# Kernel optimization log

Hardware: AMD Instinct MI355X
Metric: run time of the kernel (lower is better)

## Reference

```python
import jax, jax.numpy as jnp
import numpy as np

B, S, H = 32, 2048, 1024


def setup_inputs() -> dict:
    key = jax.random.key(0)
    k1, k2, k3, k4, k5, k6 = jax.random.split(key, 6)
    scale = 1.0 / np.sqrt(H)
    return {
        "query": jax.random.normal(k1, (B, 1, H), dtype=jnp.float32),
        "encoder_outputs": jax.random.normal(k2, (B, S, H), dtype=jnp.float32),
        "src_lengths": jax.random.randint(k3, (B,), 0, S, dtype=jnp.int64),
        "W_h": jax.random.normal(k4, (H, H), dtype=jnp.float32) * scale,
        "W_s": jax.random.normal(k5, (H, H), dtype=jnp.float32) * scale,
        "v": jax.random.normal(k6, (H,), dtype=jnp.float32) * scale,
    }


def reference(query, encoder_outputs, src_lengths, W_h, W_s, v):
    # score(h_i, s) = v^T tanh(W_h h_i + W_s s)
    proj_h = jnp.einsum("bsh,hd->bsd", encoder_outputs, W_h)   # (B,S,H)
    proj_s = jnp.einsum("bqh,hd->bqd", query, W_s)             # (B,1,H)
    scores = jnp.einsum("bsd,d->bs", jnp.tanh(proj_h + proj_s), v)  # (B,S)
    # sequence mask: True for valid positions
    mask = jnp.arange(encoder_outputs.shape[1])[None, :] < src_lengths[:, None]
    scores = jnp.where(mask, scores, -1e9)
    attn_weights = jax.nn.softmax(scores, axis=1)              # (B,S)
    attn_out = jnp.einsum("bs,bsh->bh", attn_weights, encoder_outputs)
    return attn_out[:, None, :]  # (B,1,H)
```

## Files before the change

### kernel.cpp

```cpp
#include <hip/hip_runtime.h>
#include <hip/hip_bf16.h>
#include <stdint.h>

#define NB 32
#define NS 2048
#define NH 1024

typedef __attribute__((ext_vector_type(8))) unsigned short ushort8v;
typedef __attribute__((ext_vector_type(4))) unsigned short ushort4v;
typedef __attribute__((ext_vector_type(8))) __bf16 bf16x8;
typedef __attribute__((ext_vector_type(4))) float floatx4;

__device__ __forceinline__ unsigned short f2bf(float f) {
    union { float f; unsigned int u; } x; x.f = f;
    unsigned int r = x.u + 0x7fffu + ((x.u >> 16) & 1u);
    return (unsigned short)(r >> 16);
}
__device__ __forceinline__ float bf2f(unsigned short u) {
    union { unsigned int u; float f; } x; x.u = ((unsigned int)u) << 16;
    return x.f;
}
__device__ __forceinline__ float tanh_fast(float x) {
    float e2 = __expf(2.0f * x);
    return 1.0f - 2.0f * __builtin_amdgcn_rcpf(e2 + 1.0f);
}
__device__ __forceinline__ void gload_lds16(const void* g, void* l) {
    __builtin_amdgcn_global_load_lds(
        (const __attribute__((address_space(1))) unsigned int*)g,
        (__attribute__((address_space(3))) unsigned int*)l, 16, 0, 0);
}

__global__ void prep_kernel(const float* __restrict__ E,
                            const int* __restrict__ lens,
                            unsigned short* __restrict__ Ebf,
                            const float* __restrict__ Wh,
                            unsigned short* __restrict__ WhP,
                            const float* __restrict__ q,
                            const float* __restrict__ Ws,
                            float* __restrict__ projs)
{
    const int bid = blockIdx.x;
    const int t   = threadIdx.x;
    if (bid >= 256) {
        int r = bid - 256;
        int len = lens[r >> 11];
        if (len != 0 && (r & (NS - 1)) >= len) return;
        float4 f = *(const float4*)(E + (size_t)r * NH + t * 4);
        ushort4v u;
        u[0] = f2bf(f.x); u[1] = f2bf(f.y); u[2] = f2bf(f.z); u[3] = f2bf(f.w);
        *(ushort4v*)(Ebf + (size_t)r * NH + t * 4) = u;
        return;
    }
    if (bid < 128) {
        int kb = bid;
        int n  = t * 4;
        int ni = n & 15, nh = n >> 4;
        for (int i = 0; i < 8; ++i) {
            int k = kb * 8 + i;
            float4 w = *(const float4*)(Wh + (size_t)k * NH + n);
            size_t base = (size_t)nh * 16384 + (size_t)(k >> 5) * 512 + (k & 31);
            WhP[base + (size_t)(ni + 0) * 32] = f2bf(w.x);
            WhP[base + (size_t)(ni + 1) * 32] = f2bf(w.y);
            WhP[base + (size_t)(ni + 2) * 32] = f2bf(w.z);
            WhP[base + (size_t)(ni + 3) * 32] = f2bf(w.w);
        }
        return;
    }
    {
        int lb = bid - 128;
        int b  = lb >> 2;
        int d0 = (lb & 3) * 256;
        int kg = t >> 6;
        int dc = t & 63;
        const float* qb = q + (size_t)b * NH;
        float4 acc = {0.f, 0.f, 0.f, 0.f};
        for (int k = kg * 256; k < kg * 256 + 256; ++k) {
            float qv = qb[k];
            float4 wv = *(const float4*)(Ws + (size_t)k * NH + d0 + dc * 4);
            acc.x += qv * wv.x; acc.y += qv * wv.y;
            acc.z += qv * wv.z; acc.w += qv * wv.w;
        }
        __shared__ float4 red[4][64];
        red[kg][dc] = acc;
        __syncthreads();
        if (t < 64) {
            float4 s = red[0][t];
            float4 s1 = red[1][t], s2 = red[2][t], s3 = red[3][t];
            s.x += s1.x + s2.x + s3.x; s.y += s1.y + s2.y + s3.y;
            s.z += s1.z + s2.z + s3.z; s.w += s1.w + s2.w + s3.w;
            *(float4*)(projs + (size_t)b * NH + d0 + t * 4) = s;
        }
    }
}

__global__ __launch_bounds__(512) void scores_kernel(
    const unsigned short* __restrict__ Ebf, const unsigned short* __restrict__ WhP,
    const float* __restrict__ projs, const float* __restrict__ v,
    const int* __restrict__ lens, float* __restrict__ spart)
{
    extern __shared__ __align__(16) unsigned short smem[];
    unsigned short* Al = smem;
    unsigned short* Bl = smem + 32768;
    float* sc = (float*)(smem + 65536);

    const int tid  = threadIdx.x;
    const int wgid = blockIdx.x;
    const int vid  = (wgid & 7) * 128 + (wgid >> 3);
    const int rt   = vid >> 2;
    const int cb   = vid & 3;
    const int brow = rt * 256;
    const int b    = brow >> 11;
    const int sloc = brow & (NS - 1);
    if (sloc >= lens[b]) return;

    const int wave = tid >> 6;
    const int lane = tid & 63;
    const int l15 = lane & 15;
    const int l16 = lane >> 4;
    const int wM = wave >> 2;
    const int wN = wave & 3;

    floatx4 acc[8][4];
    #pragma unroll
    for (int m = 0; m < 8; ++m)
        #pragma unroll
        for (int n = 0; n < 4; ++n) acc[m][n] = (floatx4){0.f, 0.f, 0.f, 0.f};

    const unsigned short* AsrcB = Ebf
        + (size_t)(brow + wave * 32 + (lane >> 3)) * NH
        + ((lane & 7) ^ (lane >> 3)) * 8;
    const unsigned short* BsrcB = WhP
        + (size_t)(cb * 16 + wave * 2) * 16384
        + (lane >> 2) * 32 + ((lane & 3) ^ ((lane >> 3) & 3)) * 8;

    #define STAGE(buf, kt)                                                     \
    {                                                                          \
        _Pragma("unroll")                                                      \
        for (int u = 0; u < 4; ++u)                                            \
            gload_lds16(AsrcB + (size_t)(u * 8) * NH + (kt) * 64,              \
                        (void*)&Al[(buf) * 16384 + (wave * 4 + u) * 512]);     \
        _Pragma("unroll")                                                      \
        for (int u = 0; u < 4; ++u)                                            \
            gload_lds16(BsrcB + (size_t)(u >> 1) * 16384                       \
                              + ((kt) * 2 + (u & 1)) * 512,                    \
                        (void*)&Bl[(buf) * 16384 + (wave * 4 + u) * 512]);     \
    }

    const int arow = wM * 128 + l15;
    const int asw7 = l15 & 7;
    const int bsw = (l16 ^ ((l15 >> 1) & 3)) * 8;

    #define PHASE(buf, kk)                                                     \
    {                                                                          \
        bf16x8 a[8]; bf16x8 bb[4];                                             \
        _Pragma("unroll")                                                      \
        for (int m = 0; m < 8; ++m)                                            \
            a[m] = __builtin_bit_cast(bf16x8, *(const ushort8v*)               \
                &Al[(buf) * 16384 + (arow + m * 16) * 64                       \
                    + (((kk) * 4 + l16) ^ asw7) * 8]);                         \
        _Pragma("unroll")                                                      \
        for (int n = 0; n < 4; ++n)                                            \
            bb[n] = __builtin_bit_cast(bf16x8, *(const ushort8v*)              \
                &Bl[(buf) * 16384 + ((wN * 4 + n) * 2 + (kk)) * 512            \
                    + l15 * 32 + bsw]);                                        \
        __builtin_amdgcn_s_setprio(1);                                         \
        _Pragma("unroll")                                                      \
        for (int m = 0; m < 8; ++m)                                            \
            _Pragma("unroll")                                                  \
            for (int n = 0; n < 4; ++n)                                        \
                acc[m][n] = __builtin_amdgcn_mfma_f32_16x16x32_bf16(           \
                    a[m], bb[n], acc[m][n], 0, 0, 0);                          \
        __builtin_amdgcn_s_setprio(0);                                         \
    }

    STAGE(0, 0);

    for (int kt = 0; kt < 16; ++kt) {
        const int buf = kt & 1;
        asm volatile("s_waitcnt vmcnt(0)" ::: "memory");
        __builtin_amdgcn_sched_barrier(0);
        __builtin_amdgcn_s_barrier();
        __builtin_amdgcn_sched_barrier(0);
        if (kt < 15) STAGE(buf ^ 1, kt + 1);
        PHASE(buf, 0);
        __builtin_amdgcn_s_barrier();
        __builtin_amdgcn_sched_barrier(0);
        PHASE(buf, 1);
    }
    #undef STAGE
    #undef PHASE

    float psv[4], vv[4];
    #pragma unroll
    for (int n = 0; n < 4; ++n) {
        int col = cb * 256 + wN * 64 + n * 16 + l15;
        psv[n] = projs[(size_t)b * NH + col];
        vv[n]  = v[col];
    }
    #pragma unroll
    for (int m = 0; m < 8; ++m) {
        float sp[4] = {0.f, 0.f, 0.f, 0.f};
        #pragma unroll
        for (int n = 0; n < 4; ++n)
            #pragma unroll
            for (int i = 0; i < 4; ++i)
                sp[i] += tanh_fast(acc[m][n][i] + psv[n]) * vv[n];
        #pragma unroll
        for (int i = 0; i < 4; ++i) {
            float s = sp[i];
            s += __shfl_xor(s, 1);
            s += __shfl_xor(s, 2);
            s += __shfl_xor(s, 4);
            s += __shfl_xor(s, 8);
            if (l15 == 0) sc[wN * 256 + wM * 128 + m * 16 + l16 * 4 + i] = s;
        }
    }
    __syncthreads();
    if (tid < 256) {
        float s = sc[tid] + sc[256 + tid] + sc[512 + tid] + sc[768 + tid];
        spart[(size_t)cb * (NB * NS) + brow + tid] = s;
    }
}

__global__ void attnout1_kernel(const unsigned short* __restrict__ Ebf,
                                const float* __restrict__ spart,
                                const int* __restrict__ lens,
                                float* __restrict__ part)
{
    int b  = blockIdx.x;
    int ch = blockIdx.y;
    int s0 = ch * 128;
    int t  = threadIdx.x;
    int len = lens[b];
    float* po = part + ((size_t)ch * NB + b) * NH;
    if (len > 0 && s0 >= len) {
        *(float4*)(po + t * 4) = (float4){0.f, 0.f, 0.f, 0.f};
        return;
    }
    const float* p0 = spart + (size_t)b * NS;
    float loc[8];
    float mx = -3e38f;
    #pragma unroll
    for (int i = 0; i < 8; ++i) {
        int s = t + i * 256;
        float val = -1e9f;
        if (s < len) {
            val = 0.f;
            #pragma unroll
            for (int c = 0; c < 4; ++c) val += p0[(size_t)c * (NB * NS) + s];
        }
        loc[i] = val;
        mx = fmaxf(mx, val);
    }
    #pragma unroll
    for (int m = 32; m >= 1; m >>= 1) mx = fmaxf(mx, __shfl_xor(mx, m));
    __shared__ float red[4], red2[4];
    __shared__ float wsh[128];
    int w = t >> 6;
    if ((t & 63) == 0) red[w] = mx;
    __syncthreads();
    mx = fmaxf(fmaxf(red[0], red[1]), fmaxf(red[2], red[3]));
    float sum = 0.f;
    #pragma unroll
    for (int i = 0; i < 8; ++i) sum += expf(loc[i] - mx);
    #pragma unroll
    for (int m = 32; m >= 1; m >>= 1) sum += __shfl_xor(sum, m);
    if ((t & 63) == 0) red2[w] = sum;
    __syncthreads();
    sum = red2[0] + red2[1] + red2[2] + red2[3];
    float inv = 1.f / sum;
    if (t < 128) {
        int s = s0 + t;
        float val = -1e9f;
        if (s < len) {
            val = 0.f;
            #pragma unroll
            for (int c = 0; c < 4; ++c) val += p0[(size_t)c * (NB * NS) + s];
        }
        wsh[t] = expf(val - mx) * inv;
    }
    __syncthreads();
    int h0 = t * 4;
    const unsigned short* Eb = Ebf + ((size_t)b * NS + s0) * NH + h0;
    float4 acc = {0.f, 0.f, 0.f, 0.f};
    for (int s = 0; s < 128; ++s) {
        float wv = wsh[s];
        ushort4v e = *(const ushort4v*)(Eb + (size_t)s * NH);
        acc.x += wv * bf2f(e[0]); acc.y += wv * bf2f(e[1]);
        acc.z += wv * bf2f(e[2]); acc.w += wv * bf2f(e[3]);
    }
    *(float4*)(po + h0) = acc;
}

__global__ void attnout2_kernel(const float* __restrict__ part,
                                float* __restrict__ out)
{
    int b = blockIdx.x, t = threadIdx.x;
    float4 acc = {0.f, 0.f, 0.f, 0.f};
    #pragma unroll
    for (int c = 0; c < 16; ++c) {
        float4 p = *(const float4*)(part + ((size_t)c * NB + b) * NH + t * 4);
        acc.x += p.x; acc.y += p.y; acc.z += p.z; acc.w += p.w;
    }
    *(float4*)(out + (size_t)b * NH + t * 4) = acc;
}

extern "C" void kernel_launch(void* const* d_in, const int* in_sizes, int n_in,
                              void* d_out, int out_size, void* d_ws, size_t ws_size,
                              hipStream_t stream)
{
    const float* q    = (const float*)d_in[0];
    const float* E    = (const float*)d_in[1];
    const int*   lens = (const int*)d_in[2];
    const float* Wh   = (const float*)d_in[3];
    const float* Ws   = (const float*)d_in[4];
    const float* v    = (const float*)d_in[5];
    float* out = (float*)d_out;

    float* ws     = (float*)d_ws;
    float* projs  = ws;
    float* spart  = projs + 32 * 1024;
    float* part   = spart + 4 * NB * NS;
    unsigned short* WhP = (unsigned short*)(part + 16 * NB * NH);
    unsigned short* Ebf = WhP + 1024 * 1024;

    const int smem_bytes = 132 * 1024;
    hipFuncSetAttribute((const void*)scores_kernel,
                        hipFuncAttributeMaxDynamicSharedMemorySize, smem_bytes);

    prep_kernel    <<<256 + NB * NS, 256, 0, stream>>>(E, lens, Ebf, Wh, WhP, q, Ws, projs);
    scores_kernel  <<<1024, 512, smem_bytes, stream>>>(Ebf, WhP, projs, v, lens, spart);
    attnout1_kernel<<<dim3(NB, 16), 256, 0, stream>>>(Ebf, spart, lens, part);
    attnout2_kernel<<<NB, 256, 0, stream>>>(part, out);
}
```

Before: 152.9 us.

## Switch scores GEMM to triple-buffered K=32 tiles with interleaved staging

The scores GEMM main loop moves from double-buffered K=64 tiles to triple-buffered K=32 tiles, with loads issued two iterations ahead and gated by vmcnt(4). Each iteration is split into two half-M MFMA groups, and the A and B staging for a future tile is interleaved between them. LDS use drops from 132KB to about 100KB. The aim is better latency hiding and possibly higher occupancy, at the cost of more barriers per unit of work and a new swizzle layout.

Result: slower. 157.5 us (+3.0%).

```diff
diff --git a/kernel.cpp b/kernel.cpp
--- a/kernel.cpp
+++ b/kernel.cpp
@@ -100,8 +100,8 @@
 {
     extern __shared__ __align__(16) unsigned short smem[];
     unsigned short* Al = smem;
-    unsigned short* Bl = smem + 32768;
-    float* sc = (float*)(smem + 65536);
+    unsigned short* Bl = smem + 24576;
+    float* sc = (float*)(smem + 49152);
 
     const int tid  = threadIdx.x;
     const int wgid = blockIdx.x;
@@ -126,69 +126,84 @@
         #pragma unroll
         for (int n = 0; n < 4; ++n) acc[m][n] = (floatx4){0.f, 0.f, 0.f, 0.f};
 
-    const unsigned short* AsrcB = Ebf
-        + (size_t)(brow + wave * 32 + (lane >> 3)) * NH
-        + ((lane & 7) ^ (lane >> 3)) * 8;
+    const int ssw = ((lane & 3) ^ ((lane >> 3) & 3)) * 8;
+
+    const unsigned short* AsrcA = Ebf
+        + (size_t)(brow + wave * 16 + (lane >> 2)) * NH + ssw;
     const unsigned short* BsrcB = WhP
-        + (size_t)(cb * 16 + wave * 2) * 16384
-        + (lane >> 2) * 32 + ((lane & 3) ^ ((lane >> 3) & 3)) * 8;
-
-    #define STAGE(buf, kt)                                                     \
+        + (size_t)(cb * 16 + wave) * 16384 + (lane >> 2) * 32 + ssw;
+
+    #define STAGE_A(buf, kt)                                                   \
     {                                                                          \
-        _Pragma("unroll")                                                      \
-        for (int u = 0; u < 4; ++u)                                            \
-            gload_lds16(AsrcB + (size_t)(u * 8) * NH + (kt) * 64,              \
-                        (void*)&Al[(buf) * 16384 + (wave * 4 + u) * 512]);     \
-        _Pragma("unroll")                                                      \
-        for (int u = 0; u < 4; ++u)                                            \
-            gload_lds16(BsrcB + (size_t)(u >> 1) * 16384                       \
-                              + ((kt) * 2 + (u & 1)) * 512,                    \
-                        (void*)&Bl[(buf) * 16384 + (wave * 4 + u) * 512]);     \
-    }
-
-    const int arow = wM * 128 + l15;
-    const int asw7 = l15 & 7;
-    const int bsw = (l16 ^ ((l15 >> 1) & 3)) * 8;
-
-    #define PHASE(buf, kk)                                                     \
+        gload_lds16(AsrcA + (size_t)(kt) * 32,                                 \
+                    (void*)&Al[(buf) * 8192 + wave * 512]);                    \
+        gload_lds16(AsrcA + (size_t)128 * NH + (size_t)(kt) * 32,              \
+                    (void*)&Al[(buf) * 8192 + 4096 + wave * 512]);             \
+    }
+    #define STAGE_B(buf, kt)                                                   \
     {                                                                          \
-        bf16x8 a[8]; bf16x8 bb[4];                                             \
-        _Pragma("unroll")                                                      \
-        for (int m = 0; m < 8; ++m)                                            \
-            a[m] = __builtin_bit_cast(bf16x8, *(const ushort8v*)               \
-                &Al[(buf) * 16384 + (arow + m * 16) * 64                       \
-                    + (((kk) * 4 + l16) ^ asw7) * 8]);                         \
-        _Pragma("unroll")                                                      \
-        for (int n = 0; n < 4; ++n)                                            \
-            bb[n] = __builtin_bit_cast(bf16x8, *(const ushort8v*)              \
-                &Bl[(buf) * 16384 + ((wN * 4 + n) * 2 + (kk)) * 512            \
-                    + l15 * 32 + bsw]);                                        \
-        __builtin_amdgcn_s_setprio(1);                                         \
-        _Pragma("unroll")                                                      \
-        for (int m = 0; m < 8; ++m)                                            \
-            _Pragma("unroll")                                                  \
-            for (int n = 0; n < 4; ++n)                                        \
-                acc[m][n] = __builtin_amdgcn_mfma_f32_16x16x32_bf16(           \
-                    a[m], bb[n], acc[m][n], 0, 0, 0);                          \
-        __builtin_amdgcn_s_setprio(0);                                         \
-    }
-
-    STAGE(0, 0);
-
-    for (int kt = 0; kt < 16; ++kt) {
-        const int buf = kt & 1;
-        asm volatile("s_waitcnt vmcnt(0)" ::: "memory");
+        gload_lds16(BsrcB + (size_t)(kt) * 512,                                \
+                    (void*)&Bl[(buf) * 8192 + wave * 512]);                    \
+        gload_lds16(BsrcB + (size_t)8 * 16384 + (size_t)(kt) * 512,            \
+                    (void*)&Bl[(buf) * 8192 + (8 + wave) * 512]);              \
+    }
+
+    const int aslot = (l16 ^ ((l15 >> 1) & 3)) * 8;
+    const int arow0 = wM * 128 + l15;
+
+    STAGE_A(0, 0); STAGE_B(0, 0);
+    STAGE_A(1, 1); STAGE_B(1, 1);
+
+    for (int kt = 0; kt < 32; ++kt) {
+        const int rbuf = kt % 3;
+        const int sbuf = (kt + 2) % 3;
+        if (kt < 31) { asm volatile("s_waitcnt vmcnt(4)" ::: "memory"); }
+        else         { asm volatile("s_waitcnt vmcnt(0)" ::: "memory"); }
         __builtin_amdgcn_sched_barrier(0);
         __builtin_amdgcn_s_barrier();
+
+        bf16x8 a0[4], bb[4];
+        #pragma unroll
+        for (int m = 0; m < 4; ++m)
+            a0[m] = __builtin_bit_cast(bf16x8, *(const ushort8v*)
+                &Al[rbuf * 8192 + (arow0 + m * 16) * 32 + aslot]);
+        #pragma unroll
+        for (int n = 0; n < 4; ++n)
+            bb[n] = __builtin_bit_cast(bf16x8, *(const ushort8v*)
+                &Bl[rbuf * 8192 + (wN * 4 + n) * 512 + l15 * 32 + aslot]);
+        if (kt < 30) STAGE_A(sbuf, kt + 2);
+        __builtin_amdgcn_s_barrier();
+        asm volatile("s_waitcnt lgkmcnt(0)" ::: "memory");
         __builtin_amdgcn_sched_barrier(0);
-        if (kt < 15) STAGE(buf ^ 1, kt + 1);
-        PHASE(buf, 0);
+        __builtin_amdgcn_s_setprio(1);
+        #pragma unroll
+        for (int m = 0; m < 4; ++m)
+            #pragma unroll
+            for (int n = 0; n < 4; ++n)
+                acc[m][n] = __builtin_amdgcn_mfma_f32_16x16x32_bf16(
+                    a0[m], bb[n], acc[m][n], 0, 0, 0);
+        __builtin_amdgcn_s_setprio(0);
         __builtin_amdgcn_s_barrier();
+
+        bf16x8 a1[4];
+        #pragma unroll
+        for (int m = 0; m < 4; ++m)
+            a1[m] = __builtin_bit_cast(bf16x8, *(const ushort8v*)
+                &Al[rbuf * 8192 + (arow0 + (m + 4) * 16) * 32 + aslot]);
+        if (kt < 30) STAGE_B(sbuf, kt + 2);
+        asm volatile("s_waitcnt lgkmcnt(0)" ::: "memory");
         __builtin_amdgcn_sched_barrier(0);
-        PHASE(buf, 1);
-    }
-    #undef STAGE
-    #undef PHASE
+        __builtin_amdgcn_s_setprio(1);
+        #pragma unroll
+        for (int m = 0; m < 4; ++m)
+            #pragma unroll
+            for (int n = 0; n < 4; ++n)
+                acc[m + 4][n] = __builtin_amdgcn_mfma_f32_16x16x32_bf16(
+                    a1[m], bb[n], acc[m + 4][n], 0, 0, 0);
+        __builtin_amdgcn_s_setprio(0);
+    }
+    #undef STAGE_A
+    #undef STAGE_B
 
     float psv[4], vv[4];
     #pragma unroll
@@ -324,7 +339,7 @@
     unsigned short* WhP = (unsigned short*)(part + 16 * NB * NH);
     unsigned short* Ebf = WhP + 1024 * 1024;
 
-    const int smem_bytes = 132 * 1024;
+    const int smem_bytes = 49152 * 2 + 4096;
     hipFuncSetAttribute((const void*)scores_kernel,
                         hipFuncAttributeMaxDynamicSharedMemorySize, smem_bytes);
 
```
